# Kernel optimization log

Measured on AMD Instinct MI355X. Metric: run time of the kernel, lower is better.

The kernel has to match this reference:

```python
import jax, jax.numpy as jnp
import numpy as np

N_HEADS = 16

def _ln(x, g, b, eps=1e-5):
    m = jnp.mean(x, axis=-1, keepdims=True)
    v = jnp.mean((x - m) ** 2, axis=-1, keepdims=True)
    return (x - m) / jnp.sqrt(v + eps) * g + b

def _gelu(x):
    return jax.nn.gelu(x, approximate=False)

def _forward(x, pos_embed, time_embed, Wint, bint, g1, be1, Wq, bq, Wk, bk, Wv, bv,
             Wo, bo, Wm1, bm1, Wm2, bm2, g2, be2, W5, b5, ew, g3, be3, Wf1, bf1, Wf2, bf2):
    B, T, C = x.shape
    H = N_HEADS
    dh = C // H
    # PositionTimingLayer: concat pos/time halves, linear, residual add
    fused = jnp.concatenate([pos_embed[:T], time_embed[:T]], axis=-1)  # [T, C]
    x = x + fused @ Wint.T + bint
    # MechanismAttention on norm1(x)
    h = _ln(x, g1, be1)
    q = (h @ Wq.T + bq).reshape(B, T, H, dh)
    k = (h @ Wk.T + bk).reshape(B, T, H, dh)
    v = (h @ Wv.T + bv).reshape(B, T, H, dh)
    scores = jnp.einsum('bthd,bshd->bhts', q, k) / np.float32(np.sqrt(dh))  # [B,H,T,T]
    mech = jax.nn.sigmoid(_gelu(h @ Wm1.T + bm1) @ Wm2.T + bm2)[..., 0]  # [B,T]
    scores = scores * (1.0 + mech[:, None, None, :])  # modulate along key dim
    attn = jax.nn.softmax(scores, axis=-1)
    ctx = jnp.einsum('bhts,bshd->bthd', attn, v).reshape(B, T, C)
    x = x + (ctx @ Wo.T + bo)
    # FiveElementsTransformationLayer on norm2(x)
    h2 = _ln(x, g2, be2)
    proj = jnp.einsum('bti,eoi->bteo', h2, W5) + b5  # [B,T,5,C]
    w = jax.nn.softmax(ew)
    x = x + jnp.einsum('e,bteo->bto', w, proj)
    # FFN on norm3(x)
    h3 = _ln(x, g3, be3)
    x = x + (_gelu(h3 @ Wf1.T + bf1) @ Wf2.T + bf2)
    return x, mech, w

def setup_inputs() -> dict:
    key = jax.random.key(0)
    d, dff, L, five = 1024, 4096, 1024, 5
    ks = jax.random.split(key, 32)
    s = 0.02
    r = lambda i, shape: jax.random.normal(ks[i], shape, dtype=jnp.float32) * s
    return {
        'x': jax.random.normal(ks[0], (4, L, d), dtype=jnp.float32),
        'pos_embed': r(1, (L, d // 2)), 'time_embed': r(2, (L, d // 2)),
        'Wint': r(3, (d, d)), 'bint': jnp.zeros((d,)),
        'g1': jnp.ones((d,)), 'be1': jnp.zeros((d,)),
        'Wq': r(4, (d, d)), 'bq': jnp.zeros((d,)),
        'Wk': r(5, (d, d)), 'bk': jnp.zeros((d,)),
        'Wv': r(6, (d, d)), 'bv': jnp.zeros((d,)),
        'Wo': r(7, (d, d)), 'bo': jnp.zeros((d,)),
        'Wm1': r(8, (d // 2, d)), 'bm1': jnp.zeros((d // 2,)),
        'Wm2': r(9, (1, d // 2)), 'bm2': jnp.zeros((1,)),
        'g2': jnp.ones((d,)), 'be2': jnp.zeros((d,)),
        'W5': r(10, (five, d, d)), 'b5': jnp.zeros((five, d)),
        'ew': jnp.ones((five,)) / five,
        'g3': jnp.ones((d,)), 'be3': jnp.zeros((d,)),
        'Wf1': r(11, (dff, d)), 'bf1': jnp.zeros((dff,)),
        'Wf2': r(12, (d, dff)), 'bf2': jnp.zeros((d,)),
    }

def reference(x, pos_embed, time_embed, Wint, bint, g1, be1, Wq, bq, Wk, bk, Wv, bv,
              Wo, bo, Wm1, bm1, Wm2, bm2, g2, be2, W5, b5, ew, g3, be3, Wf1, bf1, Wf2, bf2):
    return _forward(x, pos_embed, time_embed, Wint, bint, g1, be1, Wq, bq, Wk, bk, Wv, bv,
                    Wo, bo, Wm1, bm1, Wm2, bm2, g2, be2, W5, b5, ew, g3, be3, Wf1, bf1, Wf2, bf2)
```

## Files before the change

### kernel.cpp

```cpp
#include <hip/hip_runtime.h>

typedef unsigned short u16;
typedef __bf16 bf16_t;
typedef bf16_t bf16x8 __attribute__((ext_vector_type(8)));
typedef float f32x4 __attribute__((ext_vector_type(4)));

__device__ __forceinline__ u16 f2b(float f){
  unsigned u = __builtin_bit_cast(unsigned, f);
  u += 0x7fffu + ((u >> 16) & 1u);
  return (u16)(u >> 16);
}
__device__ __forceinline__ float b2f(u16 h){
  return __builtin_bit_cast(float, ((unsigned)h) << 16);
}
__device__ __forceinline__ float gelu_exact(float x){
  return 0.5f * x * (1.f + erff(x * 0.70710678118654752440f));
}
__device__ __forceinline__ void gld16(const void* g, void* l){
  __builtin_amdgcn_global_load_lds((const __attribute__((address_space(1))) unsigned int*)g,
                                   (__attribute__((address_space(3))) unsigned int*)l, 16, 0, 0);
}

__global__ void k_conv(const float* __restrict__ s, u16* __restrict__ d, int n){
  int i = (blockIdx.x * 256 + threadIdx.x) * 4;
  if (i >= n) return;
  float4 v = *(const float4*)(s + i);
  ushort4 o; o.x = f2b(v.x); o.y = f2b(v.y); o.z = f2b(v.z); o.w = f2b(v.w);
  *(ushort4*)(d + i) = o;
}

__global__ void k_w5(const float* __restrict__ W5, const float* __restrict__ b5,
                     const float* __restrict__ ew, u16* __restrict__ Wc,
                     float* __restrict__ b5c, float* __restrict__ outW){
  int gid = blockIdx.x * 256 + threadIdx.x;
  float e0 = ew[0], e1 = ew[1], e2 = ew[2], e3 = ew[3], e4 = ew[4];
  float mx = fmaxf(fmaxf(fmaxf(e0, e1), fmaxf(e2, e3)), e4);
  float x0 = expf(e0 - mx), x1 = expf(e1 - mx), x2 = expf(e2 - mx), x3 = expf(e3 - mx), x4 = expf(e4 - mx);
  float inv = 1.f / (x0 + x1 + x2 + x3 + x4);
  float w0 = x0 * inv, w1 = x1 * inv, w2 = x2 * inv, w3 = x3 * inv, w4 = x4 * inv;
  float v = w0 * W5[gid] + w1 * W5[gid + 1048576] + w2 * W5[gid + 2097152]
          + w3 * W5[gid + 3145728] + w4 * W5[gid + 4194304];
  Wc[gid] = f2b(v);
  if (gid < 1024)
    b5c[gid] = w0 * b5[gid] + w1 * b5[gid + 1024] + w2 * b5[gid + 2048]
             + w3 * b5[gid + 3072] + w4 * b5[gid + 4096];
  if (gid == 0){ outW[0] = w0; outW[1] = w1; outW[2] = w2; outW[3] = w3; outW[4] = w4; }
}

__global__ void k_fused(const float* __restrict__ pos, const float* __restrict__ tim,
                        u16* __restrict__ d){
  int i = blockIdx.x * 256 + threadIdx.x;
  int t = i >> 10, c = i & 1023;
  float v = (c < 512) ? pos[t * 512 + c] : tim[t * 512 + c - 512];
  d[i] = f2b(v);
}

__global__ void k_bqkv(const float* __restrict__ bq, const float* __restrict__ bk,
                       const float* __restrict__ bv, float* __restrict__ d){
  int i = blockIdx.x * 256 + threadIdx.x;
  if (i >= 3072) return;
  d[i] = (i < 1024) ? bq[i] : (i < 2048 ? bk[i - 1024] : bv[i - 2048]);
}

__global__ void k_xinit(const float* __restrict__ xin, const float* __restrict__ tmp,
                        float* __restrict__ x){
  int i = blockIdx.x * 256 + threadIdx.x;
  float4 a = ((const float4*)xin)[i];
  float4 b = ((const float4*)tmp)[i & 262143];
  float4 o; o.x = a.x + b.x; o.y = a.y + b.y; o.z = a.z + b.z; o.w = a.w + b.w;
  ((float4*)x)[i] = o;
}

__global__ __launch_bounds__(256) void k_ln(const float* __restrict__ x, const float* __restrict__ g,
                     const float* __restrict__ be, u16* __restrict__ out){
  int row = blockIdx.x, tid = threadIdx.x;
  int w = tid >> 6, lane = tid & 63;
  const float4 v = ((const float4*)(x + (size_t)row * 1024))[tid];
  float s1 = v.x + v.y + v.z + v.w;
  float s2 = v.x * v.x + v.y * v.y + v.z * v.z + v.w * v.w;
  for (int m = 1; m < 64; m <<= 1){ s1 += __shfl_xor(s1, m, 64); s2 += __shfl_xor(s2, m, 64); }
  __shared__ float a1[4], a2[4];
  if (!lane){ a1[w] = s1; a2[w] = s2; }
  __syncthreads();
  s1 = a1[0] + a1[1] + a1[2] + a1[3];
  s2 = a2[0] + a2[1] + a2[2] + a2[3];
  float mean = s1 * (1.f / 1024.f);
  float var  = s2 * (1.f / 1024.f) - mean * mean;
  float rstd = rsqrtf(var + 1e-5f);
  float4 gv = ((const float4*)g)[tid], bv = ((const float4*)be)[tid];
  ushort4 o;
  o.x = f2b((v.x - mean) * rstd * gv.x + bv.x);
  o.y = f2b((v.y - mean) * rstd * gv.y + bv.y);
  o.z = f2b((v.z - mean) * rstd * gv.z + bv.z);
  o.w = f2b((v.w - mean) * rstd * gv.w + bv.w);
  ((ushort4*)(out + (size_t)row * 1024))[tid] = o;
}

__global__ __launch_bounds__(256) void k_mech(const u16* __restrict__ m1, const float* __restrict__ Wm2,
                      const float* __restrict__ bm2, float* __restrict__ outMech,
                      float* __restrict__ mechf){
  int tid = threadIdx.x, w = tid >> 6, lane = tid & 63;
  int r = blockIdx.x * 4 + w;
  uint4 mv = *(const uint4*)(m1 + (size_t)r * 512 + lane * 8);
  const u16* ms = (const u16*)&mv;
  float4 w0 = ((const float4*)Wm2)[lane * 2];
  float4 w1 = ((const float4*)Wm2)[lane * 2 + 1];
  float dot = b2f(ms[0]) * w0.x + b2f(ms[1]) * w0.y + b2f(ms[2]) * w0.z + b2f(ms[3]) * w0.w
            + b2f(ms[4]) * w1.x + b2f(ms[5]) * w1.y + b2f(ms[6]) * w1.z + b2f(ms[7]) * w1.w;
  for (int m = 1; m < 64; m <<= 1) dot += __shfl_xor(dot, m, 64);
  if (lane == 0){
    float z = dot + bm2[0];
    float sig = 1.f / (1.f + expf(-z));
    outMech[r] = sig;
    mechf[r] = (1.f + sig) * 0.125f;
  }
}

template<bool GELU_, bool RES, bool OUTF_EN, bool OUTB_EN>
__global__ __launch_bounds__(256) void k_gemm(const u16* __restrict__ A, const u16* __restrict__ W,
                      const float* __restrict__ bias, const float* resid,
                      float* outF, u16* outB, int M, int N, int K){
  __shared__ u16 lA[128 * 32];
  __shared__ u16 lB[128 * 32];
  const int tid = threadIdx.x;
  const int w = tid >> 6, lane = tid & 63;
  const int lr = lane & 15, lg = lane >> 4;
  const int m0 = blockIdx.y * 128, n0 = blockIdx.x * 128;
  const int wr = (w >> 1) * 64, wc = (w & 1) * 64;

  f32x4 acc[4][4] = {};
  const char* gA = (const char*)A;
  const char* gW = (const char*)W;

  for (int k0 = 0; k0 < K; k0 += 32){
    __syncthreads();
#pragma unroll
    for (int i = 0; i < 2; ++i){
      int c = i * 256 + tid;
      gld16(gA + (((size_t)(m0 + (c >> 2)) * K + k0) * 2 + (c & 3) * 16),
            (char*)lA + i * 4096 + w * 1024);
      gld16(gW + (((size_t)(n0 + (c >> 2)) * K + k0) * 2 + (c & 3) * 16),
            (char*)lB + i * 4096 + w * 1024);
    }
    __syncthreads();
    bf16x8 af[4], wf[4];
#pragma unroll
    for (int mb = 0; mb < 4; ++mb)
      af[mb] = *reinterpret_cast<const bf16x8*>(&lA[(wr + mb * 16 + lr) * 32 + lg * 8]);
#pragma unroll
    for (int nb = 0; nb < 4; ++nb)
      wf[nb] = *reinterpret_cast<const bf16x8*>(&lB[(wc + nb * 16 + lr) * 32 + lg * 8]);
#pragma unroll
    for (int mb = 0; mb < 4; ++mb)
#pragma unroll
      for (int nb = 0; nb < 4; ++nb)
        acc[mb][nb] = __builtin_amdgcn_mfma_f32_16x16x32_bf16(af[mb], wf[nb], acc[mb][nb], 0, 0, 0);
  }

#pragma unroll
  for (int mb = 0; mb < 4; ++mb){
#pragma unroll
    for (int nb = 0; nb < 4; ++nb){
      int col = n0 + wc + nb * 16 + lr;
      float bv = bias[col];
#pragma unroll
      for (int ii = 0; ii < 4; ++ii){
        int row = m0 + wr + mb * 16 + lg * 4 + ii;
        float v = acc[mb][nb][ii] + bv;
        if (GELU_) v = gelu_exact(v);
        size_t idx = (size_t)row * N + col;
        if (RES) v += resid[idx];
        if (OUTF_EN) outF[idx] = v;
        if (OUTB_EN) outB[idx] = f2b(v);
      }
    }
  }
}

__global__ __launch_bounds__(256) void k_attn(const u16* __restrict__ qkv, const float* __restrict__ mechf,
                      u16* __restrict__ ctx){
  __shared__ u16 lk[32 * 64];
  __shared__ u16 lv[64 * 32];
  __shared__ u16 lp[4 * 16 * 32];
  __shared__ float lmf[32];
  const int tid = threadIdx.x, w = tid >> 6, lane = tid & 63;
  const int lr = lane & 15, lg = lane >> 4;
  const int b = blockIdx.z, h = blockIdx.y, q0 = blockIdx.x * 64;
  const size_t base = (size_t)b * 1024;

  bf16x8 qf[2];
  {
    const u16* qrow = qkv + (base + q0 + w * 16 + lr) * 3072 + h * 64;
    qf[0] = *(const bf16x8*)(qrow + lg * 8);
    qf[1] = *(const bf16x8*)(qrow + 32 + lg * 8);
  }
  float m_i[4], l_i[4];
  f32x4 cacc[4] = {};
#pragma unroll
  for (int i = 0; i < 4; ++i){ m_i[i] = -1e30f; l_i[i] = 0.f; }

  for (int jt = 0; jt < 1024; jt += 32){
    __syncthreads();
    {
      int rowj = tid >> 3, c0 = (tid & 7) * 8;
      const u16* src = qkv + (base + jt + rowj) * 3072 + 1024 + h * 64 + c0;
      *(uint4*)&lk[rowj * 64 + c0] = *(const uint4*)src;
      uint4 vv = *(const uint4*)(src + 1024);
      const u16* vs = (const u16*)&vv;
#pragma unroll
      for (int i = 0; i < 8; ++i) lv[(c0 + i) * 32 + rowj] = vs[i];
      if (tid < 32) lmf[tid] = mechf[base + jt + tid];
    }
    __syncthreads();

    f32x4 s[2];
#pragma unroll
    for (int kb = 0; kb < 2; ++kb){
      bf16x8 kf0 = *(const bf16x8*)&lk[(kb * 16 + lr) * 64 + lg * 8];
      bf16x8 kf1 = *(const bf16x8*)&lk[(kb * 16 + lr) * 64 + 32 + lg * 8];
      f32x4 z = {};
      z = __builtin_amdgcn_mfma_f32_16x16x32_bf16(qf[0], kf0, z, 0, 0, 0);
      z = __builtin_amdgcn_mfma_f32_16x16x32_bf16(qf[1], kf1, z, 0, 0, 0);
      float f = lmf[kb * 16 + lr];
      s[kb] = z * f;
    }
    float tm[4];
#pragma unroll
    for (int i = 0; i < 4; ++i) tm[i] = fmaxf(s[0][i], s[1][i]);
#pragma unroll
    for (int off = 1; off < 16; off <<= 1)
#pragma unroll
      for (int i = 0; i < 4; ++i) tm[i] = fmaxf(tm[i], __shfl_xor(tm[i], off, 64));
    float sc[4];
#pragma unroll
    for (int i = 0; i < 4; ++i){
      float mn = fmaxf(m_i[i], tm[i]);
      sc[i] = expf(m_i[i] - mn);
      m_i[i] = mn;
    }
#pragma unroll
    for (int kb = 0; kb < 2; ++kb)
#pragma unroll
      for (int i = 0; i < 4; ++i){
        float pv = expf(s[kb][i] - m_i[i]);
        s[kb][i] = pv;
        lp[w * 512 + (lg * 4 + i) * 32 + kb * 16 + lr] = f2b(pv);
      }
#pragma unroll
    for (int i = 0; i < 4; ++i){
      float r = s[0][i] + s[1][i];
#pragma unroll
      for (int off = 1; off < 16; off <<= 1) r += __shfl_xor(r, off, 64);
      l_i[i] = l_i[i] * sc[i] + r;
#pragma unroll
      for (int db = 0; db < 4; ++db) cacc[db][i] *= sc[i];
    }
    bf16x8 pf = *(const bf16x8*)&lp[w * 512 + lr * 32 + lg * 8];
#pragma unroll
    for (int db = 0; db < 4; ++db){
      bf16x8 vf = *(const bf16x8*)&lv[(db * 16 + lr) * 32 + lg * 8];
      cacc[db] = __builtin_amdgcn_mfma_f32_16x16x32_bf16(pf, vf, cacc[db], 0, 0, 0);
    }
  }
  size_t orow0 = base + q0 + w * 16;
#pragma unroll
  for (int db = 0; db < 4; ++db)
#pragma unroll
    for (int i = 0; i < 4; ++i)
      ctx[(orow0 + lg * 4 + i) * 1024 + h * 64 + db * 16 + lr] = f2b(cacc[db][i] / l_i[i]);
}

extern "C" void kernel_launch(void* const* d_in, const int* in_sizes, int n_in,
                              void* d_out, int out_size, void* d_ws, size_t ws_size,
                              hipStream_t stream){
  const float* x_in = (const float*)d_in[0];
  const float* pos  = (const float*)d_in[1];
  const float* tim  = (const float*)d_in[2];
  const float* Wint = (const float*)d_in[3];
  const float* bint = (const float*)d_in[4];
  const float* g1   = (const float*)d_in[5];
  const float* be1  = (const float*)d_in[6];
  const float* Wq   = (const float*)d_in[7];
  const float* bq   = (const float*)d_in[8];
  const float* Wk   = (const float*)d_in[9];
  const float* bk   = (const float*)d_in[10];
  const float* Wv   = (const float*)d_in[11];
  const float* bv   = (const float*)d_in[12];
  const float* Wo   = (const float*)d_in[13];
  const float* bo   = (const float*)d_in[14];
  const float* Wm1  = (const float*)d_in[15];
  const float* bm1  = (const float*)d_in[16];
  const float* Wm2  = (const float*)d_in[17];
  const float* bm2  = (const float*)d_in[18];
  const float* g2   = (const float*)d_in[19];
  const float* be2  = (const float*)d_in[20];
  const float* W5   = (const float*)d_in[21];
  const float* b5   = (const float*)d_in[22];
  const float* ew   = (const float*)d_in[23];
  const float* g3   = (const float*)d_in[24];
  const float* be3  = (const float*)d_in[25];
  const float* Wf1  = (const float*)d_in[26];
  const float* bf1  = (const float*)d_in[27];
  const float* Wf2  = (const float*)d_in[28];
  const float* bf2  = (const float*)d_in[29];

  float* outX = (float*)d_out;
  float* outM = outX + 4194304;
  float* outW = outX + 4198400;

  char* p = (char*)d_ws;
  auto alloc = [&](size_t bytes) -> char* {
    char* r = p; p += (bytes + 255) & ~(size_t)255; return r;
  };
  u16* Wint_b = (u16*)alloc(1048576 * 2);
  u16* Wqkv_b = (u16*)alloc(3145728 * 2);
  u16* Wm1_b  = (u16*)alloc(524288 * 2);
  u16* Wo_b   = (u16*)alloc(1048576 * 2);
  u16* Wc_b   = (u16*)alloc(1048576 * 2);
  u16* Wf1_b  = (u16*)alloc(4194304 * 2);
  u16* Wf2_b  = (u16*)alloc(4194304 * 2);
  u16* fus_b  = (u16*)alloc(1048576 * 2);
  float* bqkv = (float*)alloc(3072 * 4);
  float* b5c  = (float*)alloc(1024 * 4);
  float* mechf= (float*)alloc(4096 * 4);
  float* tmpF = (float*)alloc(1048576 * 4);
  float* xbuf = (float*)alloc(4194304 * 4);
  u16* h_b    = (u16*)alloc(4194304 * 2);
  char* big   = alloc(36 * 1024 * 1024);
  u16* qkv_b  = (u16*)big;
  u16* m1_b   = (u16*)(big + 24 * 1024 * 1024);
  u16* ctx_b  = (u16*)(big + 28 * 1024 * 1024);
  u16* f1_b   = (u16*)big;

  dim3 blk(256);
  k_conv<<<1024, blk, 0, stream>>>(Wint, Wint_b, 1048576);
  k_conv<<<1024, blk, 0, stream>>>(Wq, Wqkv_b, 1048576);
  k_conv<<<1024, blk, 0, stream>>>(Wk, Wqkv_b + 1048576, 1048576);
  k_conv<<<1024, blk, 0, stream>>>(Wv, Wqkv_b + 2097152, 1048576);
  k_conv<<<512,  blk, 0, stream>>>(Wm1, Wm1_b, 524288);
  k_conv<<<1024, blk, 0, stream>>>(Wo, Wo_b, 1048576);
  k_conv<<<4096, blk, 0, stream>>>(Wf1, Wf1_b, 4194304);
  k_conv<<<4096, blk, 0, stream>>>(Wf2, Wf2_b, 4194304);
  k_w5<<<4096, blk, 0, stream>>>(W5, b5, ew, Wc_b, b5c, outW);
  k_fused<<<4096, blk, 0, stream>>>(pos, tim, fus_b);
  k_bqkv<<<12, blk, 0, stream>>>(bq, bk, bv, bqkv);

  k_gemm<false,false,true,false><<<dim3(8, 8), blk, 0, stream>>>(
      fus_b, Wint_b, bint, nullptr, tmpF, nullptr, 1024, 1024, 1024);
  k_xinit<<<4096, blk, 0, stream>>>(x_in, tmpF, xbuf);

  k_ln<<<4096, blk, 0, stream>>>(xbuf, g1, be1, h_b);
  k_gemm<false,false,false,true><<<dim3(24, 32), blk, 0, stream>>>(
      h_b, Wqkv_b, bqkv, nullptr, nullptr, qkv_b, 4096, 3072, 1024);
  k_gemm<true,false,false,true><<<dim3(4, 32), blk, 0, stream>>>(
      h_b, Wm1_b, bm1, nullptr, nullptr, m1_b, 4096, 512, 1024);
  k_mech<<<1024, blk, 0, stream>>>(m1_b, Wm2, bm2, outM, mechf);
  k_attn<<<dim3(16, 16, 4), blk, 0, stream>>>(qkv_b, mechf, ctx_b);
  k_gemm<false,true,true,false><<<dim3(8, 32), blk, 0, stream>>>(
      ctx_b, Wo_b, bo, xbuf, xbuf, nullptr, 4096, 1024, 1024);

  k_ln<<<4096, blk, 0, stream>>>(xbuf, g2, be2, h_b);
  k_gemm<false,true,true,false><<<dim3(8, 32), blk, 0, stream>>>(
      h_b, Wc_b, b5c, xbuf, xbuf, nullptr, 4096, 1024, 1024);

  k_ln<<<4096, blk, 0, stream>>>(xbuf, g3, be3, h_b);
  k_gemm<true,false,false,true><<<dim3(32, 32), blk, 0, stream>>>(
      h_b, Wf1_b, bf1, nullptr, nullptr, f1_b, 4096, 4096, 1024);
  k_gemm<false,true,true,false><<<dim3(8, 32), blk, 0, stream>>>(
      f1_b, Wf2_b, bf2, xbuf, outX, nullptr, 4096, 1024, 4096);
}
```

Before: 680.9 us.

## Pre-transpose V and stream K/V into LDS with async loads in attention

Adds a kernel that transposes V per (batch, head) into a separate buffer, reusing the LN output buffer. The attention kernel now uses 64-key tiles loaded with global_load_lds into XOR-swizzled LDS, reads P through ds_read_b64_tr_b16, and runs two MFMAs per output block. It also switches to __expf and raises wave priority around the MFMA sections. The goal is to remove the scalar LDS scatter used for the V transpose and to halve the number of tile iterations. The cost is an extra launch and an extra pass over V in memory.

New measurement: 621.2 us. -8.8%, faster.

```diff
diff --git a/kernel.cpp b/kernel.cpp
--- a/kernel.cpp
+++ b/kernel.cpp
@@ -3,6 +3,7 @@
 typedef unsigned short u16;
 typedef __bf16 bf16_t;
 typedef bf16_t bf16x8 __attribute__((ext_vector_type(8)));
+typedef bf16_t bf16x4 __attribute__((ext_vector_type(4)));
 typedef float f32x4 __attribute__((ext_vector_type(4)));
 
 __device__ __forceinline__ u16 f2b(float f){
@@ -35,7 +36,7 @@
   int gid = blockIdx.x * 256 + threadIdx.x;
   float e0 = ew[0], e1 = ew[1], e2 = ew[2], e3 = ew[3], e4 = ew[4];
   float mx = fmaxf(fmaxf(fmaxf(e0, e1), fmaxf(e2, e3)), e4);
-  float x0 = expf(e0 - mx), x1 = expf(e1 - mx), x2 = expf(e2 - mx), x3 = expf(e3 - mx), x4 = expf(e4 - mx);
+  float x0 = __expf(e0 - mx), x1 = __expf(e1 - mx), x2 = __expf(e2 - mx), x3 = __expf(e3 - mx), x4 = __expf(e4 - mx);
   float inv = 1.f / (x0 + x1 + x2 + x3 + x4);
   float w0 = x0 * inv, w1 = x1 * inv, w2 = x2 * inv, w3 = x3 * inv, w4 = x4 * inv;
   float v = w0 * W5[gid] + w1 * W5[gid + 1048576] + w2 * W5[gid + 2097152]
@@ -110,10 +111,35 @@
   for (int m = 1; m < 64; m <<= 1) dot += __shfl_xor(dot, m, 64);
   if (lane == 0){
     float z = dot + bm2[0];
-    float sig = 1.f / (1.f + expf(-z));
+    float sig = 1.f / (1.f + __expf(-z));
     outMech[r] = sig;
     mechf[r] = (1.f + sig) * 0.125f;
   }
+}
+
+__global__ __launch_bounds__(256) void k_vt(const u16* __restrict__ qkv, u16* __restrict__ vT){
+  __shared__ u16 lt[64 * 64];
+  const int tid = threadIdx.x;
+  const int b = blockIdx.z, h = blockIdx.y, t0 = blockIdx.x * 64;
+  const size_t base = (size_t)b * 1024;
+#pragma unroll
+  for (int i = 0; i < 2; ++i){
+    int c = i * 256 + tid;
+    int r = c >> 3, ch = c & 7;
+    uint4 v = *(const uint4*)(qkv + (base + t0 + r) * 3072 + 2048 + h * 64 + ch * 8);
+    *(uint4*)((char*)lt + r * 128 + ((ch ^ (r & 7)) << 4)) = v;
+  }
+  __syncthreads();
+  int d = tid >> 2, tt = (tid & 3) * 16;
+  u16 o[16];
+#pragma unroll
+  for (int j = 0; j < 16; ++j){
+    int t = tt + j;
+    o[j] = *(const u16*)((char*)lt + t * 128 + (((d >> 3) ^ (t & 7)) << 4) + (d & 7) * 2);
+  }
+  u16* dst = vT + ((size_t)(b * 16 + h) * 64 + d) * 1024 + t0 + tt;
+  *(uint4*)dst = *(uint4*)&o[0];
+  *(uint4*)(dst + 8) = *(uint4*)&o[8];
 }
 
 template<bool GELU_, bool RES, bool OUTF_EN, bool OUTB_EN>
@@ -177,16 +203,17 @@
   }
 }
 
-__global__ __launch_bounds__(256) void k_attn(const u16* __restrict__ qkv, const float* __restrict__ mechf,
-                      u16* __restrict__ ctx){
-  __shared__ u16 lk[32 * 64];
-  __shared__ u16 lv[64 * 32];
-  __shared__ u16 lp[4 * 16 * 32];
-  __shared__ float lmf[32];
+__global__ __launch_bounds__(256) void k_attn(const u16* __restrict__ qkv, const u16* __restrict__ vT,
+                      const float* __restrict__ mechf, u16* __restrict__ ctx){
+  __shared__ u16 lk[64 * 64];
+  __shared__ u16 lvt[64 * 64];
+  __shared__ u16 lpt[4][64 * 16];
+  __shared__ float lmf[64];
   const int tid = threadIdx.x, w = tid >> 6, lane = tid & 63;
   const int lr = lane & 15, lg = lane >> 4;
   const int b = blockIdx.z, h = blockIdx.y, q0 = blockIdx.x * 64;
   const size_t base = (size_t)b * 1024;
+  const size_t bh = (size_t)(b * 16 + h);
 
   bf16x8 qf[2];
   {
@@ -199,34 +226,45 @@
 #pragma unroll
   for (int i = 0; i < 4; ++i){ m_i[i] = -1e30f; l_i[i] = 0.f; }
 
-  for (int jt = 0; jt < 1024; jt += 32){
+  char* lkb = (char*)lk;
+  char* lvb = (char*)lvt;
+  unsigned lpw = (unsigned)(uintptr_t)(__attribute__((address_space(3))) u16*)&lpt[w][0];
+  unsigned ta = lpw + lg * 256 + lr * 8;
+
+  for (int jt = 0; jt < 1024; jt += 64){
     __syncthreads();
-    {
-      int rowj = tid >> 3, c0 = (tid & 7) * 8;
-      const u16* src = qkv + (base + jt + rowj) * 3072 + 1024 + h * 64 + c0;
-      *(uint4*)&lk[rowj * 64 + c0] = *(const uint4*)src;
-      uint4 vv = *(const uint4*)(src + 1024);
-      const u16* vs = (const u16*)&vv;
-#pragma unroll
-      for (int i = 0; i < 8; ++i) lv[(c0 + i) * 32 + rowj] = vs[i];
-      if (tid < 32) lmf[tid] = mechf[base + jt + tid];
-    }
+#pragma unroll
+    for (int i = 0; i < 2; ++i){
+      int c = i * 256 + tid;
+      int row = c >> 3, ch = c & 7;
+      int chs = ch ^ (row & 7);
+      gld16(qkv + (base + jt + row) * 3072 + 1024 + h * 64 + chs * 8,
+            lkb + i * 4096 + w * 1024);
+      gld16(vT + (bh * 64 + row) * 1024 + jt + chs * 8,
+            lvb + i * 4096 + w * 1024);
+    }
+    if (tid < 64) lmf[tid] = mechf[base + jt + tid];
     __syncthreads();
 
-    f32x4 s[2];
-#pragma unroll
-    for (int kb = 0; kb < 2; ++kb){
-      bf16x8 kf0 = *(const bf16x8*)&lk[(kb * 16 + lr) * 64 + lg * 8];
-      bf16x8 kf1 = *(const bf16x8*)&lk[(kb * 16 + lr) * 64 + 32 + lg * 8];
+    f32x4 s[4];
+    __builtin_amdgcn_s_setprio(1);
+#pragma unroll
+    for (int kb = 0; kb < 4; ++kb){
+      int row = kb * 16 + lr;
+      bf16x8 kf0 = *(const bf16x8*)(lkb + row * 128 + ((lg ^ (row & 7)) << 4));
+      bf16x8 kf1 = *(const bf16x8*)(lkb + row * 128 + (((4 + lg) ^ (row & 7)) << 4));
       f32x4 z = {};
       z = __builtin_amdgcn_mfma_f32_16x16x32_bf16(qf[0], kf0, z, 0, 0, 0);
       z = __builtin_amdgcn_mfma_f32_16x16x32_bf16(qf[1], kf1, z, 0, 0, 0);
-      float f = lmf[kb * 16 + lr];
+      float f = lmf[row];
       s[kb] = z * f;
     }
+    __builtin_amdgcn_s_setprio(0);
+
     float tm[4];
 #pragma unroll
-    for (int i = 0; i < 4; ++i) tm[i] = fmaxf(s[0][i], s[1][i]);
+    for (int i = 0; i < 4; ++i)
+      tm[i] = fmaxf(fmaxf(s[0][i], s[1][i]), fmaxf(s[2][i], s[3][i]));
 #pragma unroll
     for (int off = 1; off < 16; off <<= 1)
 #pragma unroll
@@ -235,32 +273,50 @@
 #pragma unroll
     for (int i = 0; i < 4; ++i){
       float mn = fmaxf(m_i[i], tm[i]);
-      sc[i] = expf(m_i[i] - mn);
+      sc[i] = __expf(m_i[i] - mn);
       m_i[i] = mn;
     }
 #pragma unroll
-    for (int kb = 0; kb < 2; ++kb)
-#pragma unroll
-      for (int i = 0; i < 4; ++i){
-        float pv = expf(s[kb][i] - m_i[i]);
-        s[kb][i] = pv;
-        lp[w * 512 + (lg * 4 + i) * 32 + kb * 16 + lr] = f2b(pv);
-      }
+    for (int kb = 0; kb < 4; ++kb){
+      ushort4 pk;
+      float p0 = __expf(s[kb][0] - m_i[0]); s[kb][0] = p0; pk.x = f2b(p0);
+      float p1 = __expf(s[kb][1] - m_i[1]); s[kb][1] = p1; pk.y = f2b(p1);
+      float p2 = __expf(s[kb][2] - m_i[2]); s[kb][2] = p2; pk.z = f2b(p2);
+      float p3 = __expf(s[kb][3] - m_i[3]); s[kb][3] = p3; pk.w = f2b(p3);
+      *(uint2*)((char*)&lpt[w][0] + (kb * 16 + lr) * 32 + lg * 8) =
+          __builtin_bit_cast(uint2, pk);
+    }
 #pragma unroll
     for (int i = 0; i < 4; ++i){
-      float r = s[0][i] + s[1][i];
+      float r = (s[0][i] + s[1][i]) + (s[2][i] + s[3][i]);
 #pragma unroll
       for (int off = 1; off < 16; off <<= 1) r += __shfl_xor(r, off, 64);
       l_i[i] = l_i[i] * sc[i] + r;
 #pragma unroll
       for (int db = 0; db < 4; ++db) cacc[db][i] *= sc[i];
     }
-    bf16x8 pf = *(const bf16x8*)&lp[w * 512 + lr * 32 + lg * 8];
+
+    asm volatile("s_waitcnt lgkmcnt(0)" ::: "memory");
+    bf16x4 t00, t01, t10, t11;
+    asm volatile("ds_read_b64_tr_b16 %0, %1 offset:0"    : "=v"(t00) : "v"(ta));
+    asm volatile("ds_read_b64_tr_b16 %0, %1 offset:128"  : "=v"(t01) : "v"(ta));
+    asm volatile("ds_read_b64_tr_b16 %0, %1 offset:1024" : "=v"(t10) : "v"(ta));
+    asm volatile("ds_read_b64_tr_b16 %0, %1 offset:1152" : "=v"(t11) : "v"(ta));
+    asm volatile("s_waitcnt lgkmcnt(0)");
+    __builtin_amdgcn_sched_barrier(0);
+    bf16x8 pf0 = __builtin_shufflevector(t00, t01, 0, 1, 2, 3, 4, 5, 6, 7);
+    bf16x8 pf1 = __builtin_shufflevector(t10, t11, 0, 1, 2, 3, 4, 5, 6, 7);
+
+    __builtin_amdgcn_s_setprio(1);
 #pragma unroll
     for (int db = 0; db < 4; ++db){
-      bf16x8 vf = *(const bf16x8*)&lv[(db * 16 + lr) * 32 + lg * 8];
-      cacc[db] = __builtin_amdgcn_mfma_f32_16x16x32_bf16(pf, vf, cacc[db], 0, 0, 0);
-    }
+      int row = db * 16 + lr;
+      bf16x8 vf0 = *(const bf16x8*)(lvb + row * 128 + ((lg ^ (row & 7)) << 4));
+      bf16x8 vf1 = *(const bf16x8*)(lvb + row * 128 + (((4 + lg) ^ (row & 7)) << 4));
+      cacc[db] = __builtin_amdgcn_mfma_f32_16x16x32_bf16(pf0, vf0, cacc[db], 0, 0, 0);
+      cacc[db] = __builtin_amdgcn_mfma_f32_16x16x32_bf16(pf1, vf1, cacc[db], 0, 0, 0);
+    }
+    __builtin_amdgcn_s_setprio(0);
   }
   size_t orow0 = base + q0 + w * 16;
 #pragma unroll
@@ -331,6 +387,7 @@
   u16* m1_b   = (u16*)(big + 24 * 1024 * 1024);
   u16* ctx_b  = (u16*)(big + 28 * 1024 * 1024);
   u16* f1_b   = (u16*)big;
+  u16* vT_b   = h_b;
 
   dim3 blk(256);
   k_conv<<<1024, blk, 0, stream>>>(Wint, Wint_b, 1048576);
@@ -355,7 +412,8 @@
   k_gemm<true,false,false,true><<<dim3(4, 32), blk, 0, stream>>>(
       h_b, Wm1_b, bm1, nullptr, nullptr, m1_b, 4096, 512, 1024);
   k_mech<<<1024, blk, 0, stream>>>(m1_b, Wm2, bm2, outM, mechf);
-  k_attn<<<dim3(16, 16, 4), blk, 0, stream>>>(qkv_b, mechf, ctx_b);
+  k_vt<<<dim3(16, 16, 4), blk, 0, stream>>>(qkv_b, vT_b);
+  k_attn<<<dim3(16, 16, 4), blk, 0, stream>>>(qkv_b, vT_b, mechf, ctx_b);
   k_gemm<false,true,true,false><<<dim3(8, 32), blk, 0, stream>>>(
       ctx_b, Wo_b, bo, xbuf, xbuf, nullptr, 4096, 1024, 1024);
 
```
